# Kernel optimization log

Measured on AMD Instinct MI355X. Metric: run time of the kernel, lower is better.

Reference implementation:

```python
import jax, jax.numpy as jnp
import numpy as np
from jax import lax

# Module constraint: hidden_dim == state_dim == expand_dim (see broadcasting in original).
H = 128  # hidden_dim
N = 128  # state_dim
E = 128  # expand_dim = hidden_dim * expand_factor (expand_factor=1)
B, L = 4, 1024


def setup_inputs() -> dict:
    key = jax.random.key(0)
    ks = jax.random.split(key, 11)
    s = lambda fan: 1.0 / np.sqrt(fan)
    return {
        "u": jax.random.normal(ks[0], (B, L, H), jnp.float32),
        "W_in": jax.random.normal(ks[1], (H, 2 * E), jnp.float32) * s(H),
        "b_in": jax.random.normal(ks[2], (2 * E,), jnp.float32) * 0.01,
        "conv_w": jax.random.normal(ks[3], (E, 1, 3), jnp.float32) * s(3),
        "conv_b": jax.random.normal(ks[4], (E,), jnp.float32) * 0.01,
        "W_x": jax.random.normal(ks[5], (E, N + N + H), jnp.float32) * s(E),
        "b_x": jax.random.normal(ks[6], (N + N + H,), jnp.float32) * 0.01,
        "A_log": jax.random.normal(ks[7], (N,), jnp.float32),
        "D": jnp.ones((H,), jnp.float32),
        "W_out": jax.random.normal(ks[8], (E, H), jnp.float32) * s(E),
        "b_out": jax.random.normal(ks[9], (H,), jnp.float32) * 0.01,
    }


def reference(u, W_in, b_in, conv_w, conv_b, W_x, b_x, A_log, D, W_out, b_out):
    b, l, _ = u.shape
    xz = u @ W_in + b_in                       # [B,L,2E]
    x, z = jnp.split(xz, 2, axis=-1)           # [B,L,E] each
    # depthwise conv1d, kernel 3, padding 1 (groups == channels)
    xc = lax.conv_general_dilated(
        x.transpose(0, 2, 1), conv_w, window_strides=(1,), padding=[(1, 1)],
        feature_group_count=E, dimension_numbers=("NCH", "OIH", "NCH"))
    x = jax.nn.silu(xc.transpose(0, 2, 1) + conv_b)  # [B,L,E]
    ssm = x @ W_x + b_x                        # [B,L,2N+H]
    delta = jax.nn.softplus(ssm[..., :N])      # [B,L,N]
    Bm = ssm[..., N:2 * N]                     # [B,L,N]
    C = ssm[..., 2 * N:]                       # [B,L,H]
    A = -jnp.exp(A_log)                        # [N]

    def step(h, inp):
        d_t, B_t, C_t, x_t, u_t = inp          # [B,N],[B,N],[B,H],[B,E],[B,H]
        # A_discrete[b,t,i,j] = exp(delta[b,t,i] * A[j])  (outer broadcast, as in source)
        A_disc = jnp.exp(d_t[:, :, None] * A[None, None, :])       # [B,N,N]
        h = A_disc * h + (d_t * B_t)[:, :, None] * x_t[:, None, :]  # [B,N,E]
        y = (h * C_t[:, None, :]).sum(axis=1) + D * u_t             # [B,H]
        return h, y

    h0 = jnp.zeros((b, N, H), u.dtype)
    inputs = (delta.transpose(1, 0, 2), Bm.transpose(1, 0, 2),
              C.transpose(1, 0, 2), x.transpose(1, 0, 2), u.transpose(1, 0, 2))
    _, ys = lax.scan(step, h0, inputs)         # ys: [L,B,H]
    y = ys.transpose(1, 0, 2) * jax.nn.silu(z)  # [B,L,H] (E==H)
    return y @ W_out + b_out                   # dropout in eval mode: identity
```

## Files before the change

### kernel.cpp

```cpp
#include <hip/hip_runtime.h>
#include <hip/hip_bf16.h>

using bf16 = __hip_bfloat16;
typedef __attribute__((ext_vector_type(8))) short short8;
typedef __attribute__((ext_vector_type(4))) float f32x4;

#define BVAL 4
#define LVAL 1024
#define LOG2E 1.44269504f

#define TSEG 64
#define SSEG 16
#define CH   16
#define YST  72

#define OFF_U      0
#define OFF_WIN    524288
#define OFF_BIN    557056
#define OFF_CONVW  557312
#define OFF_CONVB  557696
#define OFF_WX     557824
#define OFF_BX     606976
#define OFF_ALOG   607360
#define OFF_D      607488
#define OFF_WOUT   607616
#define OFF_BOUT   624000
#define CVT_TOTAL  624128
#define FP32N      (CVT_TOTAL - OFF_WIN)

#define CVT2_U   524288
#define CVT2_WI  (CVT2_U + 32768)
#define CVT2_WX  (CVT2_WI + 49152)
#define CVT2_TOT (CVT2_WX + 16384)

__device__ __forceinline__ int dtype_flag(const void* D) {
    return ((*(const unsigned int*)D) & 0xFFFFu) != 0u ? 1 : 0;
}
__device__ __forceinline__ float ldin(const void* p, size_t i, int f) {
    return f ? __bfloat162float(((const bf16*)p)[i]) : ((const float*)p)[i];
}

__global__ void kcvt_all(const void* __restrict__ u, const void* __restrict__ W_in,
                         const void* __restrict__ b_in, const void* __restrict__ conv_w,
                         const void* __restrict__ conv_b, const void* __restrict__ W_x,
                         const void* __restrict__ b_x, const void* __restrict__ A_log,
                         const void* __restrict__ D, const void* __restrict__ W_out,
                         const void* __restrict__ b_out, float* __restrict__ dst,
                         bf16* __restrict__ ubf, bf16* __restrict__ wtin,
                         bf16* __restrict__ wtx, bf16* __restrict__ wtout) {
    int gidx = blockIdx.x * 256 + threadIdx.x;
    int f = dtype_flag(D);
    if (gidx < FP32N) {
        int idx = gidx + OFF_WIN;
        const void* p; int loc;
        if      (idx < OFF_BIN)   { p = W_in;   loc = idx - OFF_WIN; }
        else if (idx < OFF_CONVW) { p = b_in;   loc = idx - OFF_BIN; }
        else if (idx < OFF_CONVB) { p = conv_w; loc = idx - OFF_CONVW; }
        else if (idx < OFF_WX)    { p = conv_b; loc = idx - OFF_CONVB; }
        else if (idx < OFF_BX)    { p = W_x;    loc = idx - OFF_WX; }
        else if (idx < OFF_ALOG)  { p = b_x;    loc = idx - OFF_BX; }
        else if (idx < OFF_D)     { p = A_log;  loc = idx - OFF_ALOG; }
        else if (idx < OFF_WOUT)  { p = D;      loc = idx - OFF_D; }
        else if (idx < OFF_BOUT)  { p = W_out;  loc = idx - OFF_WOUT; }
        else                      { p = b_out;  loc = idx - OFF_BOUT; }
        dst[idx] = ldin(p, loc, f);
    } else {
        int ix = gidx - FP32N;
        if (ix >= CVT2_TOT) return;
        if (ix < CVT2_U) {
            ubf[ix] = __float2bfloat16(ldin(u, ix, f));
        } else if (ix < CVT2_WI) {
            int rel = ix - CVT2_U; int n = rel >> 7, k = rel & 127;
            wtin[rel] = __float2bfloat16(ldin(W_in, k * 256 + n, f));
        } else if (ix < CVT2_WX) {
            int rel = ix - CVT2_WI; int n = rel >> 7, k = rel & 127;
            wtx[rel] = __float2bfloat16(ldin(W_x, k * 384 + n, f));
        } else {
            int rel = ix - CVT2_WX; int n = rel >> 7, k = rel & 127;
            wtout[rel] = __float2bfloat16(ldin(W_out, k * 128 + n, f));
        }
    }
}

__global__ void k1_mfma(const bf16* __restrict__ ubf, const bf16* __restrict__ wtin,
                        const float* __restrict__ cvt,
                        float* __restrict__ x_pre, bf16* __restrict__ zsbf) {
    int blk = blockIdx.x, mb = blk >> 3, cb = blk & 7;
    int tid = threadIdx.x, w = tid >> 6, lane = tid & 63;
    int quad = lane >> 4, sub = lane & 15;
    int m0 = mb * 64 + w * 16, c = cb * 16;
    f32x4 accX = {0.f, 0.f, 0.f, 0.f}, accZ = {0.f, 0.f, 0.f, 0.f};
    #pragma unroll
    for (int ks = 0; ks < 4; ++ks) {
        int k0 = ks * 32 + quad * 8;
        short8 a  = *(const short8*)(ubf + (size_t)(m0 + sub) * 128 + k0);
        short8 bX = *(const short8*)(wtin + (size_t)(c + sub) * 128 + k0);
        short8 bZ = *(const short8*)(wtin + (size_t)(128 + c + sub) * 128 + k0);
        accX = __builtin_amdgcn_mfma_f32_16x16x32_bf16(a, bX, accX, 0, 0, 0);
        accZ = __builtin_amdgcn_mfma_f32_16x16x32_bf16(a, bZ, accZ, 0, 0, 0);
    }
    int o = c + sub;
    float bx_ = cvt[OFF_BIN + o], bz_ = cvt[OFF_BIN + 128 + o];
    #pragma unroll
    for (int r = 0; r < 4; ++r) {
        int m = m0 + quad * 4 + r;
        float x = accX[r] + bx_;
        float z = accZ[r] + bz_;
        x_pre[(size_t)m * 128 + o] = x;
        zsbf[(size_t)m * 128 + o] = __float2bfloat16(z / (1.0f + __expf(-z)));
    }
}

__global__ void k2_conv(const float* __restrict__ cvt, const float* __restrict__ x_pre,
                        float* __restrict__ xs, bf16* __restrict__ xsbf) {
    const float* conv_w = cvt + OFF_CONVW;
    const float* conv_b = cvt + OFF_CONVB;
    int q = blockIdx.x * 256 + threadIdx.x;
    int basee = q * 4;
    int row = basee >> 7;
    int l = row & (LVAL - 1);
    int e = basee & 127;
    float4 xc = *(const float4*)(x_pre + basee);
    float4 xm = make_float4(0.f, 0.f, 0.f, 0.f);
    float4 xp = make_float4(0.f, 0.f, 0.f, 0.f);
    if (l > 0)        xm = *(const float4*)(x_pre + basee - 128);
    if (l < LVAL - 1) xp = *(const float4*)(x_pre + basee + 128);
    float mm[4] = {xm.x, xm.y, xm.z, xm.w};
    float cc[4] = {xc.x, xc.y, xc.z, xc.w};
    float pp[4] = {xp.x, xp.y, xp.z, xp.w};
    float out[4];
    #pragma unroll
    for (int i = 0; i < 4; ++i) {
        float w0 = conv_w[(e + i) * 3 + 0];
        float w1 = conv_w[(e + i) * 3 + 1];
        float w2 = conv_w[(e + i) * 3 + 2];
        float v = fmaf(w0, mm[i], fmaf(w1, cc[i], fmaf(w2, pp[i], conv_b[e + i])));
        out[i] = v / (1.0f + __expf(-v));
    }
    *(float4*)(xs + basee) = make_float4(out[0], out[1], out[2], out[3]);
    #pragma unroll
    for (int i = 0; i < 4; ++i) xsbf[basee + i] = __float2bfloat16(out[i]);
}

__global__ void k3_mfma(const bf16* __restrict__ xsbf, const bf16* __restrict__ wtx,
                        const float* __restrict__ cvt,
                        float* __restrict__ delta, float* __restrict__ dB,
                        float* __restrict__ Cc) {
    int blk = blockIdx.x, mb = blk >> 3, cb = blk & 7;
    int tid = threadIdx.x, w = tid >> 6, lane = tid & 63;
    int quad = lane >> 4, sub = lane & 15;
    int m0 = mb * 64 + w * 16, c = cb * 16;
    f32x4 accA = {0.f,0.f,0.f,0.f}, accB = {0.f,0.f,0.f,0.f}, accC = {0.f,0.f,0.f,0.f};
    #pragma unroll
    for (int ks = 0; ks < 4; ++ks) {
        int k0 = ks * 32 + quad * 8;
        short8 a  = *(const short8*)(xsbf + (size_t)(m0 + sub) * 128 + k0);
        short8 bA = *(const short8*)(wtx + (size_t)(c + sub) * 128 + k0);
        short8 bB = *(const short8*)(wtx + (size_t)(128 + c + sub) * 128 + k0);
        short8 bC = *(const short8*)(wtx + (size_t)(256 + c + sub) * 128 + k0);
        accA = __builtin_amdgcn_mfma_f32_16x16x32_bf16(a, bA, accA, 0, 0, 0);
        accB = __builtin_amdgcn_mfma_f32_16x16x32_bf16(a, bB, accB, 0, 0, 0);
        accC = __builtin_amdgcn_mfma_f32_16x16x32_bf16(a, bC, accC, 0, 0, 0);
    }
    int o = c + sub;
    float ba = cvt[OFF_BX + o], bb = cvt[OFF_BX + 128 + o], bc = cvt[OFF_BX + 256 + o];
    #pragma unroll
    for (int r = 0; r < 4; ++r) {
        int m = m0 + quad * 4 + r;
        size_t idx = (size_t)m * 128 + o;
        float d = accA[r] + ba;
        float sp = (d > 20.0f) ? d : log1pf(__expf(d));
        delta[idx] = sp;
        dB[idx] = sp * (accB[r] + bb);
        Cc[idx] = accC[r] + bc;
    }
}


__global__ __launch_bounds__(256, 4)
void k5a(const float* __restrict__ cvt, const float* __restrict__ delta,
         const float* __restrict__ dB, const float* __restrict__ xs,
         float* __restrict__ hout, float* __restrict__ Pout) {
    __shared__ float sx[TSEG][8];
    int blk = blockIdx.x;
    int b = blk >> 8, s = (blk >> 4) & 15, jg = blk & 15;
    int tid = threadIdx.x, w = tid >> 6, lane = tid & 63;
    int cj = lane >> 5, ln = lane & 31;
    int jj = w * 2 + cj, j = jg * 8 + jj;
    int t0 = s * TSEG;
    size_t base = (size_t)b * (LVAL * 128);
    #pragma unroll
    for (int i = 0; i < 2; ++i) {
        int q = i * 256 + tid;
        int t = q >> 3, jc = q & 7;
        sx[t][jc] = xs[base + (size_t)(t0 + t) * 128 + jg * 8 + jc];
    }
    __syncthreads();
    float a2 = -__expf(cvt[OFF_ALOG + j]) * LOG2E;
    const float4* dp = (const float4*)(delta + base) + (size_t)t0 * 32 + ln;
    const float4* wp = (const float4*)(dB + base) + (size_t)t0 * 32 + ln;
    float h[4] = {0.f, 0.f, 0.f, 0.f};
    float sd[4] = {0.f, 0.f, 0.f, 0.f};
    for (int c4 = 0; c4 < 4; ++c4) {
        #pragma unroll 4
        for (int k = 0; k < CH; ++k) {
            int t = c4 * CH + k;
            float4 d  = dp[(size_t)t * 32];
            float4 wv = wp[(size_t)t * 32];
            float xv = sx[t][jj];
            float e;
            e = exp2f(d.x * a2); h[0] = fmaf(e, h[0], wv.x * xv); sd[0] += d.x;
            e = exp2f(d.y * a2); h[1] = fmaf(e, h[1], wv.y * xv); sd[1] += d.y;
            e = exp2f(d.z * a2); h[2] = fmaf(e, h[2], wv.z * xv); sd[2] += d.z;
            e = exp2f(d.w * a2); h[3] = fmaf(e, h[3], wv.w * xv); sd[3] += d.w;
        }
        __syncthreads();
    }
    size_t cb = (((size_t)(b * SSEG + s) * 128 + j) * 128) + 4 * ln;
    *(float4*)(hout + cb) = make_float4(h[0], h[1], h[2], h[3]);
    *(float4*)(Pout + cb) = make_float4(exp2f(sd[0] * a2), exp2f(sd[1] * a2),
                                        exp2f(sd[2] * a2), exp2f(sd[3] * a2));
}

__global__ __launch_bounds__(256, 4)
void k5c(const float* __restrict__ cvt, const float* __restrict__ delta,
         const float* __restrict__ dB, const float* __restrict__ Cc,
         const float* __restrict__ xs, const bf16* __restrict__ zsbf,
         const void* __restrict__ uin, const void* __restrict__ Din,
         const float* __restrict__ hout, const float* __restrict__ Pout,
         bf16* __restrict__ y2bf) {
    __shared__ float sx[TSEG][8], sc[TSEG][8], su[TSEG][8], sz[TSEG][8];
    __shared__ float yt[4][CH * YST];
    __shared__ float sy[TSEG][9];
    int blk = blockIdx.x;
    int b = blk >> 8, s = (blk >> 4) & 15, jg = blk & 15;
    int tid = threadIdx.x, w = tid >> 6, lane = tid & 63;
    int cj = lane >> 5, ln = lane & 31;
    int jj = w * 2 + cj, j = jg * 8 + jj;
    int t0 = s * TSEG;
    int f = dtype_flag(Din);
    size_t base = (size_t)b * (LVAL * 128);
    #pragma unroll
    for (int i = 0; i < 2; ++i) {
        int q = i * 256 + tid;
        int t = q >> 3, jc = q & 7;
        size_t g = base + (size_t)(t0 + t) * 128 + jg * 8 + jc;
        sx[t][jc] = xs[g];
        sc[t][jc] = Cc[g];
        su[t][jc] = ldin(uin, g, f);
        sz[t][jc] = __bfloat162float(zsbf[g]);
    }
    __syncthreads();
    float a2 = -__expf(cvt[OFF_ALOG + j]) * LOG2E;
    float Dj = cvt[OFF_D + j];
    float h[4] = {0.f, 0.f, 0.f, 0.f};
    size_t cstep = (size_t)128 * 128;
    size_t cb0 = (((size_t)(b * SSEG) * 128 + j) * 128) + 4 * ln;
    for (int sp = 0; sp < s; ++sp) {
        size_t cb = cb0 + (size_t)sp * cstep;
        float4 ho = *(const float4*)(hout + cb);
        float4 pp = *(const float4*)(Pout + cb);
        h[0] = fmaf(pp.x, h[0], ho.x); h[1] = fmaf(pp.y, h[1], ho.y);
        h[2] = fmaf(pp.z, h[2], ho.z); h[3] = fmaf(pp.w, h[3], ho.w);
    }
    const float4* dp = (const float4*)(delta + base) + (size_t)t0 * 32 + ln;
    const float4* wp = (const float4*)(dB + base) + (size_t)t0 * 32 + ln;
    float* ytw = yt[w];
    int rk = lane & 15, rc2 = lane >> 5, rhl = (lane >> 4) & 1;
    for (int c4 = 0; c4 < 4; ++c4) {
        #pragma unroll 4
        for (int k = 0; k < CH; ++k) {
            int t = c4 * CH + k;
            float4 d  = dp[(size_t)t * 32];
            float4 wv = wp[(size_t)t * 32];
            float xv = sx[t][jj];
            float e;
            e = exp2f(d.x * a2); h[0] = fmaf(e, h[0], wv.x * xv);
            e = exp2f(d.y * a2); h[1] = fmaf(e, h[1], wv.y * xv);
            e = exp2f(d.z * a2); h[2] = fmaf(e, h[2], wv.z * xv);
            e = exp2f(d.w * a2); h[3] = fmaf(e, h[3], wv.w * xv);
            ytw[k * YST + cj * 36 + ln] = (h[0] + h[1]) + (h[2] + h[3]);
        }
        __builtin_amdgcn_wave_barrier();
        {
            const float* rowp = &ytw[rk * YST + rc2 * 36 + rhl * 16];
            float4 v0 = *(const float4*)(rowp + 0);
            float4 v1 = *(const float4*)(rowp + 4);
            float4 v2 = *(const float4*)(rowp + 8);
            float4 v3 = *(const float4*)(rowp + 12);
            float sm = (((v0.x + v0.y) + (v0.z + v0.w)) + ((v1.x + v1.y) + (v1.z + v1.w)))
                     + (((v2.x + v2.y) + (v2.z + v2.w)) + ((v3.x + v3.y) + (v3.z + v3.w)));
            sm += __shfl_xor(sm, 16, 64);
            if (rhl == 0) {
                int t = c4 * CH + rk;
                int jj2 = w * 2 + rc2;
                float y = fmaf(sc[t][jj2], sm, Dj * su[t][jj2]);
                sy[t][jj2] = y * sz[t][jj2];
            }
        }
        __syncthreads();
    }
    #pragma unroll
    for (int i = 0; i < 2; ++i) {
        int q = i * 256 + tid;
        int t = q >> 3, jc = q & 7;
        y2bf[base + (size_t)(t0 + t) * 128 + jg * 8 + jc] = __float2bfloat16(sy[t][jc]);
    }
}

__global__ void k6_mfma(const bf16* __restrict__ y2bf, const bf16* __restrict__ wtout,
                        const float* __restrict__ cvt, const void* __restrict__ Din,
                        void* __restrict__ out) {
    int blk = blockIdx.x, mb = blk >> 2, nb = blk & 3;
    int tid = threadIdx.x, w = tid >> 6, lane = tid & 63;
    int quad = lane >> 4, sub = lane & 15;
    int m0 = mb * 64 + w * 16, n0 = nb * 32;
    f32x4 acc0 = {0.f,0.f,0.f,0.f}, acc1 = {0.f,0.f,0.f,0.f};
    #pragma unroll
    for (int ks = 0; ks < 4; ++ks) {
        int k0 = ks * 32 + quad * 8;
        short8 a  = *(const short8*)(y2bf + (size_t)(m0 + sub) * 128 + k0);
        short8 b0 = *(const short8*)(wtout + (size_t)(n0 + sub) * 128 + k0);
        short8 b1 = *(const short8*)(wtout + (size_t)(n0 + 16 + sub) * 128 + k0);
        acc0 = __builtin_amdgcn_mfma_f32_16x16x32_bf16(a, b0, acc0, 0, 0, 0);
        acc1 = __builtin_amdgcn_mfma_f32_16x16x32_bf16(a, b1, acc1, 0, 0, 0);
    }
    int f = dtype_flag(Din);
    float bo0 = cvt[OFF_BOUT + n0 + sub], bo1 = cvt[OFF_BOUT + n0 + 16 + sub];
    #pragma unroll
    for (int r = 0; r < 4; ++r) {
        int m = m0 + quad * 4 + r;
        float v0 = acc0[r] + bo0, v1 = acc1[r] + bo1;
        if (f) {
            ((bf16*)out)[(size_t)m * 128 + n0 + sub] = __float2bfloat16(v0);
            ((bf16*)out)[(size_t)m * 128 + n0 + 16 + sub] = __float2bfloat16(v1);
        } else {
            ((float*)out)[(size_t)m * 128 + n0 + sub] = v0;
            ((float*)out)[(size_t)m * 128 + n0 + 16 + sub] = v1;
        }
    }
}

extern "C" void kernel_launch(void* const* d_in, const int* in_sizes, int n_in,
                              void* d_out, int out_size, void* d_ws, size_t ws_size,
                              hipStream_t stream) {
    const size_t NE = (size_t)BVAL * LVAL * 128;
    const size_t NC = (size_t)BVAL * SSEG * 128 * 128;

    float* cvt   = (float*)d_ws;
    float* bufs  = cvt + CVT_TOTAL;
    float* x_pre = bufs + 0 * NE;
    float* zsb   = bufs + 1 * NE;
    float* xs    = bufs + 2 * NE;
    float* delta = bufs + 3 * NE;
    float* dB    = bufs + 4 * NE;
    float* Cc    = bufs + 5 * NE;
    float* hout  = bufs + 6 * NE;
    float* Pou   = hout + NC;
    float* bfarea = Pou + NC;
    bf16* zsbf  = (bf16*)zsb;
    bf16* ubf   = (bf16*)bfarea;
    bf16* xsbf  = ubf + NE;
    bf16* y2bf  = xsbf + NE;
    bf16* wtin  = y2bf + NE;
    bf16* wtx   = wtin + 32768;
    bf16* wtout = wtx + 49152;

    const int ROWS = BVAL * LVAL;
    const int CVT_ALL = FP32N + CVT2_TOT;

    kcvt_all<<<(CVT_ALL + 255) / 256, 256, 0, stream>>>(
        d_in[0], d_in[1], d_in[2], d_in[3], d_in[4], d_in[5],
        d_in[6], d_in[7], d_in[8], d_in[9], d_in[10],
        cvt, ubf, wtin, wtx, wtout);
    k1_mfma<<<512, 256, 0, stream>>>(ubf, wtin, cvt, x_pre, zsbf);
    k2_conv<<<(ROWS * 128) / (256 * 4), 256, 0, stream>>>(cvt, x_pre, xs, xsbf);
    k3_mfma<<<512, 256, 0, stream>>>(xsbf, wtx, cvt, delta, dB, Cc);
    k5a<<<BVAL * SSEG * 16, 256, 0, stream>>>(cvt, delta, dB, xs, hout, Pou);
    k5c<<<BVAL * SSEG * 16, 256, 0, stream>>>(cvt, delta, dB, Cc, xs, zsbf,
                                              d_in[0], d_in[8], hout, Pou, y2bf);
    k6_mfma<<<256, 256, 0, stream>>>(y2bf, wtout, cvt, d_in[8], d_out);
}
```

Measured before the change: 170.9 us.

## Pack delta and dB as bf16 pairs, stage scan inputs through LDS

Stores delta and delta*B as one packed 32-bit word of two bf16 values, and stores C, xs and the y staging buffers in bf16 instead of fp32. This roughly halves the global traffic the two scan kernels read from L2/HBM. Those kernels now load each 32-step chunk of packed data into shared memory with coalesced copies, instead of strided float4 loads per step. The y reduction is reworked to 8-step groups. Lower precision in delta feeds the exponent of the decay term and may add error across the recurrence.

```diff
diff --git a/kernel.cpp b/kernel.cpp
--- a/kernel.cpp
+++ b/kernel.cpp
@@ -11,10 +11,8 @@
 
 #define TSEG 64
 #define SSEG 16
-#define CH   16
 #define YST  72
 
-#define OFF_U      0
 #define OFF_WIN    524288
 #define OFF_BIN    557056
 #define OFF_CONVW  557312
@@ -39,6 +37,18 @@
 __device__ __forceinline__ float ldin(const void* p, size_t i, int f) {
     return f ? __bfloat162float(((const bf16*)p)[i]) : ((const float*)p)[i];
 }
+__device__ __forceinline__ unsigned int bfbits(float f) {
+    bf16 h = __float2bfloat16(f);
+    unsigned short s; __builtin_memcpy(&s, &h, 2);
+    return (unsigned int)s;
+}
+__device__ __forceinline__ float hi_f(unsigned int u) {
+    unsigned int v = u & 0xFFFF0000u; float f; __builtin_memcpy(&f, &v, 4); return f;
+}
+__device__ __forceinline__ float lo_f(unsigned int u) {
+    unsigned int v = u << 16; float f; __builtin_memcpy(&f, &v, 4); return f;
+}
+__device__ __forceinline__ float b2f(bf16 v) { return __bfloat162float(v); }
 
 __global__ void kcvt_all(const void* __restrict__ u, const void* __restrict__ W_in,
                          const void* __restrict__ b_in, const void* __restrict__ conv_w,
@@ -112,7 +122,7 @@
 }
 
 __global__ void k2_conv(const float* __restrict__ cvt, const float* __restrict__ x_pre,
-                        float* __restrict__ xs, bf16* __restrict__ xsbf) {
+                        bf16* __restrict__ xsbf) {
     const float* conv_w = cvt + OFF_CONVW;
     const float* conv_b = cvt + OFF_CONVB;
     int q = blockIdx.x * 256 + threadIdx.x;
@@ -128,24 +138,19 @@
     float mm[4] = {xm.x, xm.y, xm.z, xm.w};
     float cc[4] = {xc.x, xc.y, xc.z, xc.w};
     float pp[4] = {xp.x, xp.y, xp.z, xp.w};
-    float out[4];
     #pragma unroll
     for (int i = 0; i < 4; ++i) {
         float w0 = conv_w[(e + i) * 3 + 0];
         float w1 = conv_w[(e + i) * 3 + 1];
         float w2 = conv_w[(e + i) * 3 + 2];
         float v = fmaf(w0, mm[i], fmaf(w1, cc[i], fmaf(w2, pp[i], conv_b[e + i])));
-        out[i] = v / (1.0f + __expf(-v));
-    }
-    *(float4*)(xs + basee) = make_float4(out[0], out[1], out[2], out[3]);
-    #pragma unroll
-    for (int i = 0; i < 4; ++i) xsbf[basee + i] = __float2bfloat16(out[i]);
+        xsbf[basee + i] = __float2bfloat16(v / (1.0f + __expf(-v)));
+    }
 }
 
 __global__ void k3_mfma(const bf16* __restrict__ xsbf, const bf16* __restrict__ wtx,
                         const float* __restrict__ cvt,
-                        float* __restrict__ delta, float* __restrict__ dB,
-                        float* __restrict__ Cc) {
+                        unsigned int* __restrict__ dw, bf16* __restrict__ Cbf) {
     int blk = blockIdx.x, mb = blk >> 3, cb = blk & 7;
     int tid = threadIdx.x, w = tid >> 6, lane = tid & 63;
     int quad = lane >> 4, sub = lane & 15;
@@ -170,18 +175,18 @@
         size_t idx = (size_t)m * 128 + o;
         float d = accA[r] + ba;
         float sp = (d > 20.0f) ? d : log1pf(__expf(d));
-        delta[idx] = sp;
-        dB[idx] = sp * (accB[r] + bb);
-        Cc[idx] = accC[r] + bc;
+        dw[idx] = (bfbits(sp) << 16) | bfbits(sp * (accB[r] + bb));
+        Cbf[idx] = __float2bfloat16(accC[r] + bc);
     }
 }
 
 
 __global__ __launch_bounds__(256, 4)
-void k5a(const float* __restrict__ cvt, const float* __restrict__ delta,
-         const float* __restrict__ dB, const float* __restrict__ xs,
+void k5a(const float* __restrict__ cvt, const unsigned int* __restrict__ dw,
+         const bf16* __restrict__ xsbf,
          float* __restrict__ hout, float* __restrict__ Pout) {
-    __shared__ float sx[TSEG][8];
+    __shared__ uint4 sdw[32 * 32];
+    __shared__ bf16 sxb[TSEG][8];
     int blk = blockIdx.x;
     int b = blk >> 8, s = (blk >> 4) & 15, jg = blk & 15;
     int tid = threadIdx.x, w = tid >> 6, lane = tid & 63;
@@ -193,26 +198,26 @@
     for (int i = 0; i < 2; ++i) {
         int q = i * 256 + tid;
         int t = q >> 3, jc = q & 7;
-        sx[t][jc] = xs[base + (size_t)(t0 + t) * 128 + jg * 8 + jc];
-    }
-    __syncthreads();
+        sxb[t][jc] = xsbf[base + (size_t)(t0 + t) * 128 + jg * 8 + jc];
+    }
     float a2 = -__expf(cvt[OFF_ALOG + j]) * LOG2E;
-    const float4* dp = (const float4*)(delta + base) + (size_t)t0 * 32 + ln;
-    const float4* wp = (const float4*)(dB + base) + (size_t)t0 * 32 + ln;
+    const uint4* gdw = (const uint4*)(dw + base);
     float h[4] = {0.f, 0.f, 0.f, 0.f};
     float sd[4] = {0.f, 0.f, 0.f, 0.f};
-    for (int c4 = 0; c4 < 4; ++c4) {
-        #pragma unroll 4
-        for (int k = 0; k < CH; ++k) {
-            int t = c4 * CH + k;
-            float4 d  = dp[(size_t)t * 32];
-            float4 wv = wp[(size_t)t * 32];
-            float xv = sx[t][jj];
+    for (int c2 = 0; c2 < 2; ++c2) {
+        int fb = (t0 + c2 * 32) * 32;
+        #pragma unroll
+        for (int r = 0; r < 4; ++r) sdw[r * 256 + tid] = gdw[fb + r * 256 + tid];
+        __syncthreads();
+        #pragma unroll 8
+        for (int k = 0; k < 32; ++k) {
+            uint4 pv = sdw[k * 32 + ln];
+            float xv = b2f(sxb[c2 * 32 + k][jj]);
             float e;
-            e = exp2f(d.x * a2); h[0] = fmaf(e, h[0], wv.x * xv); sd[0] += d.x;
-            e = exp2f(d.y * a2); h[1] = fmaf(e, h[1], wv.y * xv); sd[1] += d.y;
-            e = exp2f(d.z * a2); h[2] = fmaf(e, h[2], wv.z * xv); sd[2] += d.z;
-            e = exp2f(d.w * a2); h[3] = fmaf(e, h[3], wv.w * xv); sd[3] += d.w;
+            e = exp2f(hi_f(pv.x) * a2); h[0] = fmaf(e, h[0], lo_f(pv.x) * xv); sd[0] += hi_f(pv.x);
+            e = exp2f(hi_f(pv.y) * a2); h[1] = fmaf(e, h[1], lo_f(pv.y) * xv); sd[1] += hi_f(pv.y);
+            e = exp2f(hi_f(pv.z) * a2); h[2] = fmaf(e, h[2], lo_f(pv.z) * xv); sd[2] += hi_f(pv.z);
+            e = exp2f(hi_f(pv.w) * a2); h[3] = fmaf(e, h[3], lo_f(pv.w) * xv); sd[3] += hi_f(pv.w);
         }
         __syncthreads();
     }
@@ -223,15 +228,15 @@
 }
 
 __global__ __launch_bounds__(256, 4)
-void k5c(const float* __restrict__ cvt, const float* __restrict__ delta,
-         const float* __restrict__ dB, const float* __restrict__ Cc,
-         const float* __restrict__ xs, const bf16* __restrict__ zsbf,
-         const void* __restrict__ uin, const void* __restrict__ Din,
-         const float* __restrict__ hout, const float* __restrict__ Pout,
-         bf16* __restrict__ y2bf) {
-    __shared__ float sx[TSEG][8], sc[TSEG][8], su[TSEG][8], sz[TSEG][8];
-    __shared__ float yt[4][CH * YST];
-    __shared__ float sy[TSEG][9];
+void k5c(const float* __restrict__ cvt, const unsigned int* __restrict__ dw,
+         const bf16* __restrict__ Cbf, const bf16* __restrict__ xsbf,
+         const bf16* __restrict__ zsbf, const void* __restrict__ uin,
+         const void* __restrict__ Din, const float* __restrict__ hout,
+         const float* __restrict__ Pout, bf16* __restrict__ y2bf) {
+    __shared__ uint4 sdw[32 * 32];
+    __shared__ bf16 sxb[TSEG][8], scb[TSEG][8], sub_[TSEG][8], szb[TSEG][8];
+    __shared__ float yt[4][8 * YST];
+    __shared__ bf16 syb[TSEG][10];
     int blk = blockIdx.x;
     int b = blk >> 8, s = (blk >> 4) & 15, jg = blk & 15;
     int tid = threadIdx.x, w = tid >> 6, lane = tid & 63;
@@ -245,12 +250,11 @@
         int q = i * 256 + tid;
         int t = q >> 3, jc = q & 7;
         size_t g = base + (size_t)(t0 + t) * 128 + jg * 8 + jc;
-        sx[t][jc] = xs[g];
-        sc[t][jc] = Cc[g];
-        su[t][jc] = ldin(uin, g, f);
-        sz[t][jc] = __bfloat162float(zsbf[g]);
-    }
-    __syncthreads();
+        sxb[t][jc] = xsbf[g];
+        scb[t][jc] = Cbf[g];
+        szb[t][jc] = zsbf[g];
+        sub_[t][jc] = __float2bfloat16(ldin(uin, g, f));
+    }
     float a2 = -__expf(cvt[OFF_ALOG + j]) * LOG2E;
     float Dj = cvt[OFF_D + j];
     float h[4] = {0.f, 0.f, 0.f, 0.f};
@@ -263,40 +267,43 @@
         h[0] = fmaf(pp.x, h[0], ho.x); h[1] = fmaf(pp.y, h[1], ho.y);
         h[2] = fmaf(pp.z, h[2], ho.z); h[3] = fmaf(pp.w, h[3], ho.w);
     }
-    const float4* dp = (const float4*)(delta + base) + (size_t)t0 * 32 + ln;
-    const float4* wp = (const float4*)(dB + base) + (size_t)t0 * 32 + ln;
+    const uint4* gdw = (const uint4*)(dw + base);
     float* ytw = yt[w];
-    int rk = lane & 15, rc2 = lane >> 5, rhl = (lane >> 4) & 1;
-    for (int c4 = 0; c4 < 4; ++c4) {
-        #pragma unroll 4
-        for (int k = 0; k < CH; ++k) {
-            int t = c4 * CH + k;
-            float4 d  = dp[(size_t)t * 32];
-            float4 wv = wp[(size_t)t * 32];
-            float xv = sx[t][jj];
-            float e;
-            e = exp2f(d.x * a2); h[0] = fmaf(e, h[0], wv.x * xv);
-            e = exp2f(d.y * a2); h[1] = fmaf(e, h[1], wv.y * xv);
-            e = exp2f(d.z * a2); h[2] = fmaf(e, h[2], wv.z * xv);
-            e = exp2f(d.w * a2); h[3] = fmaf(e, h[3], wv.w * xv);
-            ytw[k * YST + cj * 36 + ln] = (h[0] + h[1]) + (h[2] + h[3]);
-        }
-        __builtin_amdgcn_wave_barrier();
-        {
-            const float* rowp = &ytw[rk * YST + rc2 * 36 + rhl * 16];
-            float4 v0 = *(const float4*)(rowp + 0);
-            float4 v1 = *(const float4*)(rowp + 4);
-            float4 v2 = *(const float4*)(rowp + 8);
-            float4 v3 = *(const float4*)(rowp + 12);
-            float sm = (((v0.x + v0.y) + (v0.z + v0.w)) + ((v1.x + v1.y) + (v1.z + v1.w)))
-                     + (((v2.x + v2.y) + (v2.z + v2.w)) + ((v3.x + v3.y) + (v3.z + v3.w)));
-            sm += __shfl_xor(sm, 16, 64);
-            if (rhl == 0) {
-                int t = c4 * CH + rk;
-                int jj2 = w * 2 + rc2;
-                float y = fmaf(sc[t][jj2], sm, Dj * su[t][jj2]);
-                sy[t][jj2] = y * sz[t][jj2];
+    int rk = lane & 7, rc = (lane >> 3) & 1, rq = lane >> 4;
+    for (int c2 = 0; c2 < 2; ++c2) {
+        int fb = (t0 + c2 * 32) * 32;
+        #pragma unroll
+        for (int r = 0; r < 4; ++r) sdw[r * 256 + tid] = gdw[fb + r * 256 + tid];
+        __syncthreads();
+        for (int c8 = 0; c8 < 4; ++c8) {
+            #pragma unroll
+            for (int k = 0; k < 8; ++k) {
+                int kk = c8 * 8 + k;
+                uint4 pv = sdw[kk * 32 + ln];
+                float xv = b2f(sxb[c2 * 32 + kk][jj]);
+                float e;
+                e = exp2f(hi_f(pv.x) * a2); h[0] = fmaf(e, h[0], lo_f(pv.x) * xv);
+                e = exp2f(hi_f(pv.y) * a2); h[1] = fmaf(e, h[1], lo_f(pv.y) * xv);
+                e = exp2f(hi_f(pv.z) * a2); h[2] = fmaf(e, h[2], lo_f(pv.z) * xv);
+                e = exp2f(hi_f(pv.w) * a2); h[3] = fmaf(e, h[3], lo_f(pv.w) * xv);
+                ytw[k * YST + cj * 36 + ln] = (h[0] + h[1]) + (h[2] + h[3]);
             }
+            __builtin_amdgcn_wave_barrier();
+            {
+                const float* rowp = &ytw[rk * YST + rc * 36 + rq * 8];
+                float4 v0 = *(const float4*)(rowp + 0);
+                float4 v1 = *(const float4*)(rowp + 4);
+                float sm = ((v0.x + v0.y) + (v0.z + v0.w)) + ((v1.x + v1.y) + (v1.z + v1.w));
+                sm += __shfl_xor(sm, 16, 64);
+                sm += __shfl_xor(sm, 32, 64);
+                if (rq == 0) {
+                    int t = c2 * 32 + c8 * 8 + rk;
+                    int jj2 = w * 2 + rc;
+                    float y = fmaf(b2f(scb[t][jj2]), sm, Dj * b2f(sub_[t][jj2]));
+                    syb[t][jj2] = __float2bfloat16(y * b2f(szb[t][jj2]));
+                }
+            }
+            __builtin_amdgcn_wave_barrier();
         }
         __syncthreads();
     }
@@ -304,7 +311,7 @@
     for (int i = 0; i < 2; ++i) {
         int q = i * 256 + tid;
         int t = q >> 3, jc = q & 7;
-        y2bf[base + (size_t)(t0 + t) * 128 + jg * 8 + jc] = __float2bfloat16(sy[t][jc]);
+        y2bf[base + (size_t)(t0 + t) * 128 + jg * 8 + jc] = syb[t][jc];
     }
 }
 
@@ -350,15 +357,13 @@
     float* cvt   = (float*)d_ws;
     float* bufs  = cvt + CVT_TOTAL;
     float* x_pre = bufs + 0 * NE;
-    float* zsb   = bufs + 1 * NE;
-    float* xs    = bufs + 2 * NE;
-    float* delta = bufs + 3 * NE;
-    float* dB    = bufs + 4 * NE;
-    float* Cc    = bufs + 5 * NE;
-    float* hout  = bufs + 6 * NE;
+    unsigned int* dw = (unsigned int*)(bufs + 1 * NE);
+    float* zslot = bufs + 2 * NE;
+    float* hout  = bufs + 3 * NE;
     float* Pou   = hout + NC;
     float* bfarea = Pou + NC;
-    bf16* zsbf  = (bf16*)zsb;
+    bf16* zsbf  = (bf16*)zslot;
+    bf16* Cbf   = zsbf + NE;
     bf16* ubf   = (bf16*)bfarea;
     bf16* xsbf  = ubf + NE;
     bf16* y2bf  = xsbf + NE;
@@ -374,10 +379,10 @@
         d_in[6], d_in[7], d_in[8], d_in[9], d_in[10],
         cvt, ubf, wtin, wtx, wtout);
     k1_mfma<<<512, 256, 0, stream>>>(ubf, wtin, cvt, x_pre, zsbf);
-    k2_conv<<<(ROWS * 128) / (256 * 4), 256, 0, stream>>>(cvt, x_pre, xs, xsbf);
-    k3_mfma<<<512, 256, 0, stream>>>(xsbf, wtx, cvt, delta, dB, Cc);
-    k5a<<<BVAL * SSEG * 16, 256, 0, stream>>>(cvt, delta, dB, xs, hout, Pou);
-    k5c<<<BVAL * SSEG * 16, 256, 0, stream>>>(cvt, delta, dB, Cc, xs, zsbf,
+    k2_conv<<<(ROWS * 128) / (256 * 4), 256, 0, stream>>>(cvt, x_pre, xsbf);
+    k3_mfma<<<512, 256, 0, stream>>>(xsbf, wtx, cvt, dw, Cbf);
+    k5a<<<BVAL * SSEG * 16, 256, 0, stream>>>(cvt, dw, xsbf, hout, Pou);
+    k5c<<<BVAL * SSEG * 16, 256, 0, stream>>>(cvt, dw, Cbf, xsbf, zsbf,
                                               d_in[0], d_in[8], hout, Pou, y2bf);
     k6_mfma<<<256, 256, 0, stream>>>(y2bf, wtout, cvt, d_in[8], d_out);
 }
```

Result: faster. 159.9 us (-6.4%).
